# Kernel tuning notes

Measured on AMD Instinct MI355X. Metric: run time of the kernel, lower is better.

Reference implementation:

```python
import jax, jax.numpy as jnp
import numpy as np

DIM = 1024
N_HEADS = 16
HEAD_DIM = DIM // N_HEADS


def setup_inputs() -> dict:
    key = jax.random.key(0)
    ks = jax.random.split(key, 6)
    s = DIM ** -0.5
    return {
        "x": jax.random.normal(ks[0], (2, 2048, DIM), dtype=jnp.float32),
        "Wq": jax.random.normal(ks[1], (DIM, DIM), dtype=jnp.float32) * s,
        "Wk": jax.random.normal(ks[2], (DIM, DIM), dtype=jnp.float32) * s,
        "Wv": jax.random.normal(ks[3], (DIM, DIM), dtype=jnp.float32) * s,
        "Wo": jax.random.normal(ks[4], (DIM, DIM), dtype=jnp.float32) * s,
        "bo": jax.random.normal(ks[5], (DIM,), dtype=jnp.float32) * 0.01,
    }


def reference(x, Wq, Wk, Wv, Wo, bo):
    B, T, C = x.shape
    H, D = N_HEADS, HEAD_DIM
    # Linear(dim, dim, bias=False): y = x @ W^T
    q = (x @ Wq.T).reshape(B, T, H, D).transpose(0, 2, 1, 3)  # B H T D
    k = (x @ Wk.T).reshape(B, T, H, D).transpose(0, 2, 1, 3)
    v = (x @ Wv.T).reshape(B, T, H, D).transpose(0, 2, 1, 3)
    q = q * (D ** -0.5)
    attn = jnp.einsum('bhqd,bhkd->bhqk', q, k)  # B H T T
    causal_mask = jnp.triu(jnp.ones((T, T), dtype=bool), k=1)
    attn = jnp.where(causal_mask, -jnp.inf, attn)
    attn = jax.nn.softmax(attn, axis=-1)
    out = jnp.einsum('bhqk,bhkd->bhqd', attn, v)  # B H T D
    out = out.transpose(0, 2, 1, 3).reshape(B, T, C)
    return out @ Wo.T + bo
```

## Files before the change

### kernel.cpp

```cpp
#include <hip/hip_runtime.h>

typedef __attribute__((ext_vector_type(8))) short bf16x8;
typedef __attribute__((ext_vector_type(4))) float f32x4;

__device__ __forceinline__ ushort f2bf(float f) {
  union { float f; unsigned u; } v; v.f = f;
  unsigned r = v.u + 0x7fffu + ((v.u >> 16) & 1u);
  return (ushort)(r >> 16);
}

__device__ __forceinline__ void g2l16(const void* g, void* l) {
  __builtin_amdgcn_global_load_lds((const __attribute__((address_space(1))) unsigned*)g,
                                   (__attribute__((address_space(3))) unsigned*)l, 16, 0, 0);
}

__global__ __launch_bounds__(256) void cast_x_kernel(const float* __restrict__ x,
                                                     ushort* __restrict__ o, int n4) {
  int i = blockIdx.x * 256 + threadIdx.x;
  if (i >= n4) return;
  float4 v = ((const float4*)x)[i];
  ushort4 u; u.x = f2bf(v.x); u.y = f2bf(v.y); u.z = f2bf(v.z); u.w = f2bf(v.w);
  ((ushort4*)o)[i] = u;
}

__global__ __launch_bounds__(256) void cast_w_kernel(const float* __restrict__ Wq,
                                                     const float* __restrict__ Wk,
                                                     const float* __restrict__ Wv,
                                                     const float* __restrict__ Wo,
                                                     ushort* __restrict__ o) {
  int i = blockIdx.x * 256 + threadIdx.x;
  int row = i >> 8;
  int sel = row >> 10;
  const float* src = (sel == 0) ? Wq : (sel == 1) ? Wk : (sel == 2) ? Wv : Wo;
  float scale = (sel == 0) ? 0.125f : 1.0f;
  float4 v = ((const float4*)src)[i & 0x3FFFF];
  ushort4 u;
  u.x = f2bf(v.x * scale); u.y = f2bf(v.y * scale);
  u.z = f2bf(v.z * scale); u.w = f2bf(v.w * scale);
  ((ushort4*)o)[i] = u;
}

template<bool BF16_OUT, bool BIAS, bool SPLIT>
__global__ __launch_bounds__(256) void gemm_bt(const ushort* __restrict__ A,
                                               const ushort* __restrict__ B,
                                               void* __restrict__ Cout,
                                               const float* __restrict__ bias,
                                               int M, int N, int K) {
  __shared__ __align__(16) ushort As[128 * 32];
  __shared__ __align__(16) ushort Bs[128 * 32];
  const int m0 = blockIdx.y * 128, n0 = blockIdx.x * 128;
  const int tid = threadIdx.x, lane = tid & 63, wid = tid >> 6;
  const int quad = lane >> 4, lc = lane & 15;
  const int wm = (wid >> 1) * 64, wn = (wid & 1) * 64;
  f32x4 acc[4][4] = {};

  const int r0 = wid * 32 + (lane >> 2);
  const int c0 = (lane & 3) * 8;
  const ushort* Ag = A + (size_t)(m0 + r0) * K + c0;
  const ushort* Bg = B + (size_t)(n0 + r0) * K + c0;
  ushort* Al = &As[wid * 1024];
  ushort* Bl = &Bs[wid * 1024];

  for (int k0 = 0; k0 < K; k0 += 32) {
    __syncthreads();
    g2l16(Ag + k0, Al);
    g2l16(Ag + (size_t)16 * K + k0, Al + 512);
    g2l16(Bg + k0, Bl);
    g2l16(Bg + (size_t)16 * K + k0, Bl + 512);
    __syncthreads();

    bf16x8 af[4], bfr[4];
#pragma unroll
    for (int t = 0; t < 4; t++) {
      af[t]  = *(const bf16x8*)&As[(wm + t * 16 + lc) * 32 + quad * 8];
      bfr[t] = *(const bf16x8*)&Bs[(wn + t * 16 + lc) * 32 + quad * 8];
    }
#pragma unroll
    for (int mt = 0; mt < 4; mt++)
#pragma unroll
      for (int nt = 0; nt < 4; nt++)
        acc[mt][nt] = __builtin_amdgcn_mfma_f32_16x16x32_bf16(af[mt], bfr[nt], acc[mt][nt], 0, 0, 0);
  }

#pragma unroll
  for (int mt = 0; mt < 4; mt++) {
#pragma unroll
    for (int r = 0; r < 4; r++) {
      int row = m0 + wm + mt * 16 + quad * 4 + r;
#pragma unroll
      for (int nt = 0; nt < 4; nt++) {
        int col = n0 + wn + nt * 16 + lc;
        float v = acc[mt][nt][r];
        if (BIAS) v += bias[col];
        size_t dst;
        if (SPLIT) dst = ((size_t)(col >> 10) << 22) + (size_t)row * 1024 + (col & 1023);
        else       dst = (size_t)row * N + col;
        if (BF16_OUT) ((ushort*)Cout)[dst] = f2bf(v);
        else          ((float*)Cout)[dst]  = v;
      }
    }
  }
}

__global__ __launch_bounds__(256) void transpose_v(const ushort* __restrict__ Vb,
                                                   ushort* __restrict__ Vt) {
  __shared__ ushort tile[64][72];
  const int bh = blockIdx.y, b = bh >> 4, h = bh & 15;
  const int tt = blockIdx.x;
  const int tid = threadIdx.x;
#pragma unroll
  for (int i = 0; i < 2; i++) {
    int idx = i * 256 + tid;
    int trow = idx >> 3;
    int dcol = (idx & 7) * 8;
    uint4 v = *(const uint4*)(Vb + (size_t)(b * 2048 + tt * 64 + trow) * 1024 + h * 64 + dcol);
    ushort e[8]; *(uint4*)e = v;
#pragma unroll
    for (int j = 0; j < 8; j++) tile[dcol + j][trow] = e[j];
  }
  __syncthreads();
#pragma unroll
  for (int i = 0; i < 2; i++) {
    int idx = i * 256 + tid;
    int drow = idx >> 3;
    int tloc = (idx & 7) * 8;
    uint4 v = *(const uint4*)&tile[drow][tloc];
    *(uint4*)(Vt + (size_t)bh * 131072 + (size_t)drow * 2048 + tt * 64 + tloc) = v;
  }
}

__global__ __launch_bounds__(256) void attn_kernel(const ushort* __restrict__ Qb,
                                                   const ushort* __restrict__ Kb,
                                                   const ushort* __restrict__ Vt,
                                                   ushort* __restrict__ Out) {
  __shared__ __align__(16) ushort Ks[2][64 * 32];
  __shared__ __align__(16) ushort Vs[2][64 * 32];
  __shared__ __align__(16) ushort Ps[4][16][72];

  const int bh = blockIdx.y, b = bh >> 4, h = bh & 15;
  const int qb_block = (int)(gridDim.x - 1 - blockIdx.x) * 64;
  const int tid = threadIdx.x, lane = tid & 63, wid = tid >> 6;
  const int quad = lane >> 4, lc = lane & 15;
  const int qb = qb_block + wid * 16;

  const ushort* Qp = Qb + (size_t)(b * 2048 + qb + lc) * 1024 + h * 64;
  bf16x8 qf0 = *(const bf16x8*)(Qp + quad * 8);
  bf16x8 qf1 = *(const bf16x8*)(Qp + 32 + quad * 8);

  f32x4 o_acc[4] = {};
  float l_r[4] = {0.f, 0.f, 0.f, 0.f};

  const int lrow = lane >> 2, lcol = (lane & 3) * 8;
  const size_t kbase = (size_t)(b * 2048) * 1024 + h * 64;
  const size_t vbase = (size_t)bh * 131072;

  const int ntiles = (qb_block >> 6) + 1;
  for (int kt = 0; kt < ntiles; kt++) {
    const int kb = kt * 64;
    __syncthreads();
#pragma unroll
    for (int cc = 0; cc < 2; cc++) {
      int ck = wid + cc * 4;
      int half = ck >> 2, rg = ck & 3;
      const ushort* gK = Kb + kbase + (size_t)(kb + rg * 16 + lrow) * 1024 + half * 32 + lcol;
      g2l16(gK, &Ks[half][rg * 512]);
      const ushort* gV = Vt + vbase + (size_t)(rg * 16 + lrow) * 2048 + kb + half * 32 + lcol;
      g2l16(gV, &Vs[half][rg * 512]);
    }
    __syncthreads();

    f32x4 s[4];
#pragma unroll
    for (int c = 0; c < 4; c++) {
      bf16x8 kf0 = *(const bf16x8*)&Ks[0][(c * 16 + lc) * 32 + quad * 8];
      bf16x8 kf1 = *(const bf16x8*)&Ks[1][(c * 16 + lc) * 32 + quad * 8];
      f32x4 z = {};
      z = __builtin_amdgcn_mfma_f32_16x16x32_bf16(qf0, kf0, z, 0, 0, 0);
      z = __builtin_amdgcn_mfma_f32_16x16x32_bf16(qf1, kf1, z, 0, 0, 0);
      s[c] = z;
    }

    if (kb + 63 > qb) {
#pragma unroll
      for (int c = 0; c < 4; c++)
#pragma unroll
        for (int r = 0; r < 4; r++) {
          if (kb + c * 16 + lc > qb + quad * 4 + r) s[c][r] = -1e30f;
        }
    }

#pragma unroll
    for (int c = 0; c < 4; c++)
#pragma unroll
      for (int r = 0; r < 4; r++) {
        float p = __expf(s[c][r]);
        l_r[r] += p;
        Ps[wid][quad * 4 + r][c * 16 + lc] = f2bf(p);
      }
    __asm__ volatile("s_waitcnt lgkmcnt(0)" ::: "memory");
    bf16x8 ap0 = *(const bf16x8*)&Ps[wid][lc][quad * 8];
    bf16x8 ap1 = *(const bf16x8*)&Ps[wid][lc][32 + quad * 8];

#pragma unroll
    for (int nt = 0; nt < 4; nt++) {
      bf16x8 vb0 = *(const bf16x8*)&Vs[0][(nt * 16 + lc) * 32 + quad * 8];
      bf16x8 vb1 = *(const bf16x8*)&Vs[1][(nt * 16 + lc) * 32 + quad * 8];
      o_acc[nt] = __builtin_amdgcn_mfma_f32_16x16x32_bf16(ap0, vb0, o_acc[nt], 0, 0, 0);
      o_acc[nt] = __builtin_amdgcn_mfma_f32_16x16x32_bf16(ap1, vb1, o_acc[nt], 0, 0, 0);
    }
  }

#pragma unroll
  for (int r = 0; r < 4; r++) {
    float s_ = l_r[r];
    s_ += __shfl_xor(s_, 1);
    s_ += __shfl_xor(s_, 2);
    s_ += __shfl_xor(s_, 4);
    s_ += __shfl_xor(s_, 8);
    l_r[r] = 1.0f / s_;
  }
#pragma unroll
  for (int r = 0; r < 4; r++) {
    size_t orow = ((size_t)(b * 2048) + qb + quad * 4 + r) * 1024 + h * 64 + lc;
#pragma unroll
    for (int nt = 0; nt < 4; nt++)
      Out[orow + nt * 16] = f2bf(o_acc[nt][r] * l_r[r]);
  }
}

extern "C" void kernel_launch(void* const* d_in, const int* in_sizes, int n_in,
                              void* d_out, int out_size, void* d_ws, size_t ws_size,
                              hipStream_t stream) {
  const float* x  = (const float*)d_in[0];
  const float* Wq = (const float*)d_in[1];
  const float* Wk = (const float*)d_in[2];
  const float* Wv = (const float*)d_in[3];
  const float* Wo = (const float*)d_in[4];
  const float* bo = (const float*)d_in[5];
  float* out = (float*)d_out;

  char* ws = (char*)d_ws;
  ushort* xbf  = (ushort*)(ws);
  ushort* wcat = (ushort*)(ws + (8ull  << 20));
  ushort* qkv  = (ushort*)(ws + (16ull << 20));
  ushort* Vt   = (ushort*)(ws);
  ushort* Qp   = qkv;
  ushort* Kp   = qkv + (1ull << 22);
  ushort* Vp   = qkv + (2ull << 22);
  ushort* attn_out = Vp;

  cast_x_kernel<<<4096, 256, 0, stream>>>(x, xbf, 1048576);
  cast_w_kernel<<<4096, 256, 0, stream>>>(Wq, Wk, Wv, Wo, wcat);

  gemm_bt<true, false, true><<<dim3(24, 32), 256, 0, stream>>>(
      xbf, wcat, qkv, nullptr, 4096, 3072, 1024);

  transpose_v<<<dim3(32, 32), 256, 0, stream>>>(Vp, Vt);

  attn_kernel<<<dim3(32, 32), 256, 0, stream>>>(Qp, Kp, Vt, attn_out);

  gemm_bt<false, true, false><<<dim3(8, 32), 256, 0, stream>>>(
      attn_out, wcat + (size_t)3072 * 1024, out, bo, 4096, 1024, 1024);
}
```

Before: 224.1 us.

## Double-buffer GEMM and attention loads, widen attention q-tile, use exp2

GEMM now double-buffers its LDS tiles so the next K-slice loads while MFMAs run, and the output projection uses a 128x64 tile to launch more blocks. Attention processes 128 query rows per block (32 per wave), double-buffers K/V tiles, balances causal work by interleaving short and long blocks, and folds log2(e) into the Wq scale so the kernel can use exp2f. bf16 rounding is simplified to round-half-up, which slightly changes numerics. Double buffering has only one barrier per iteration, so correctness depends on the async load into the other buffer being ordered behind that barrier.

```diff
diff --git a/kernel.cpp b/kernel.cpp
--- a/kernel.cpp
+++ b/kernel.cpp
@@ -1,12 +1,12 @@
 #include <hip/hip_runtime.h>
+#include <math.h>
 
 typedef __attribute__((ext_vector_type(8))) short bf16x8;
 typedef __attribute__((ext_vector_type(4))) float f32x4;
 
 __device__ __forceinline__ ushort f2bf(float f) {
   union { float f; unsigned u; } v; v.f = f;
-  unsigned r = v.u + 0x7fffu + ((v.u >> 16) & 1u);
-  return (ushort)(r >> 16);
+  return (ushort)((v.u + 0x8000u) >> 16);
 }
 
 __device__ __forceinline__ void g2l16(const void* g, void* l) {
@@ -32,7 +32,7 @@
   int row = i >> 8;
   int sel = row >> 10;
   const float* src = (sel == 0) ? Wq : (sel == 1) ? Wk : (sel == 2) ? Wv : Wo;
-  float scale = (sel == 0) ? 0.125f : 1.0f;
+  float scale = (sel == 0) ? 0.125f * 1.44269504088896f : 1.0f;
   float4 v = ((const float4*)src)[i & 0x3FFFF];
   ushort4 u;
   u.x = f2bf(v.x * scale); u.y = f2bf(v.y * scale);
@@ -40,50 +40,60 @@
   ((ushort4*)o)[i] = u;
 }
 
-template<bool BF16_OUT, bool BIAS, bool SPLIT>
+template<int BN, bool BF16_OUT, bool BIAS, bool SPLIT>
 __global__ __launch_bounds__(256) void gemm_bt(const ushort* __restrict__ A,
                                                const ushort* __restrict__ B,
                                                void* __restrict__ Cout,
                                                const float* __restrict__ bias,
                                                int M, int N, int K) {
-  __shared__ __align__(16) ushort As[128 * 32];
-  __shared__ __align__(16) ushort Bs[128 * 32];
-  const int m0 = blockIdx.y * 128, n0 = blockIdx.x * 128;
+  __shared__ __align__(16) ushort As[2][128 * 32];
+  __shared__ __align__(16) ushort Bs[2][BN * 32];
+  const int m0 = blockIdx.y * 128, n0 = blockIdx.x * BN;
   const int tid = threadIdx.x, lane = tid & 63, wid = tid >> 6;
   const int quad = lane >> 4, lc = lane & 15;
-  const int wm = (wid >> 1) * 64, wn = (wid & 1) * 64;
-  f32x4 acc[4][4] = {};
-
-  const int r0 = wid * 32 + (lane >> 2);
-  const int c0 = (lane & 3) * 8;
-  const ushort* Ag = A + (size_t)(m0 + r0) * K + c0;
-  const ushort* Bg = B + (size_t)(n0 + r0) * K + c0;
-  ushort* Al = &As[wid * 1024];
-  ushort* Bl = &Bs[wid * 1024];
-
+  const int lrow = lane >> 2, lcol = (lane & 3) * 8;
+  const int wm = (BN == 128) ? (wid >> 1) * 64 : wid * 32;
+  const int wn = (BN == 128) ? (wid & 1) * 64 : 0;
+  constexpr int MT = (BN == 128) ? 4 : 2;
+
+  f32x4 acc[MT][4] = {};
+
+  auto stage = [&](int k0, int nb) {
+    const ushort* Ag = A + (size_t)(m0 + wid * 32 + lrow) * K + k0 + lcol;
+    g2l16(Ag, &As[nb][wid * 1024]);
+    g2l16(Ag + (size_t)16 * K, &As[nb][wid * 1024 + 512]);
+    if constexpr (BN == 128) {
+      const ushort* Bg = B + (size_t)(n0 + wid * 32 + lrow) * K + k0 + lcol;
+      g2l16(Bg, &Bs[nb][wid * 1024]);
+      g2l16(Bg + (size_t)16 * K, &Bs[nb][wid * 1024 + 512]);
+    } else {
+      const ushort* Bg = B + (size_t)(n0 + wid * 16 + lrow) * K + k0 + lcol;
+      g2l16(Bg, &Bs[nb][wid * 512]);
+    }
+  };
+
+  stage(0, 0);
   for (int k0 = 0; k0 < K; k0 += 32) {
+    const int nb = (k0 >> 5) & 1;
     __syncthreads();
-    g2l16(Ag + k0, Al);
-    g2l16(Ag + (size_t)16 * K + k0, Al + 512);
-    g2l16(Bg + k0, Bl);
-    g2l16(Bg + (size_t)16 * K + k0, Bl + 512);
-    __syncthreads();
-
-    bf16x8 af[4], bfr[4];
-#pragma unroll
-    for (int t = 0; t < 4; t++) {
-      af[t]  = *(const bf16x8*)&As[(wm + t * 16 + lc) * 32 + quad * 8];
-      bfr[t] = *(const bf16x8*)&Bs[(wn + t * 16 + lc) * 32 + quad * 8];
-    }
-#pragma unroll
-    for (int mt = 0; mt < 4; mt++)
+    if (k0 + 32 < K) stage(k0 + 32, nb ^ 1);
+
+    bf16x8 af[MT], bfr[4];
+#pragma unroll
+    for (int t = 0; t < MT; t++)
+      af[t] = *(const bf16x8*)&As[nb][(wm + t * 16 + lc) * 32 + quad * 8];
+#pragma unroll
+    for (int t = 0; t < 4; t++)
+      bfr[t] = *(const bf16x8*)&Bs[nb][(wn + t * 16 + lc) * 32 + quad * 8];
+#pragma unroll
+    for (int mt = 0; mt < MT; mt++)
 #pragma unroll
       for (int nt = 0; nt < 4; nt++)
         acc[mt][nt] = __builtin_amdgcn_mfma_f32_16x16x32_bf16(af[mt], bfr[nt], acc[mt][nt], 0, 0, 0);
   }
 
 #pragma unroll
-  for (int mt = 0; mt < 4; mt++) {
+  for (int mt = 0; mt < MT; mt++) {
 #pragma unroll
     for (int r = 0; r < 4; r++) {
       int row = m0 + wm + mt * 16 + quad * 4 + r;
@@ -129,103 +139,114 @@
   }
 }
 
-__global__ __launch_bounds__(256) void attn_kernel(const ushort* __restrict__ Qb,
-                                                   const ushort* __restrict__ Kb,
-                                                   const ushort* __restrict__ Vt,
-                                                   ushort* __restrict__ Out) {
-  __shared__ __align__(16) ushort Ks[2][64 * 32];
-  __shared__ __align__(16) ushort Vs[2][64 * 32];
-  __shared__ __align__(16) ushort Ps[4][16][72];
+__global__ __launch_bounds__(256, 2) void attn_kernel(const ushort* __restrict__ Qb,
+                                                      const ushort* __restrict__ Kb,
+                                                      const ushort* __restrict__ Vt,
+                                                      ushort* __restrict__ Out) {
+  __shared__ __align__(16) ushort Ks[2][2][64 * 32];
+  __shared__ __align__(16) ushort Vs[2][2][64 * 32];
+  __shared__ __align__(16) ushort Ps[4][32][72];
 
   const int bh = blockIdx.y, b = bh >> 4, h = bh & 15;
-  const int qb_block = (int)(gridDim.x - 1 - blockIdx.x) * 64;
+  const int bx = blockIdx.x;
+  const int ord = (bx & 1) ? (bx >> 1) : (15 - (bx >> 1));
+  const int qb_block = ord * 128;
   const int tid = threadIdx.x, lane = tid & 63, wid = tid >> 6;
   const int quad = lane >> 4, lc = lane & 15;
-  const int qb = qb_block + wid * 16;
-
-  const ushort* Qp = Qb + (size_t)(b * 2048 + qb + lc) * 1024 + h * 64;
-  bf16x8 qf0 = *(const bf16x8*)(Qp + quad * 8);
-  bf16x8 qf1 = *(const bf16x8*)(Qp + 32 + quad * 8);
-
-  f32x4 o_acc[4] = {};
-  float l_r[4] = {0.f, 0.f, 0.f, 0.f};
-
   const int lrow = lane >> 2, lcol = (lane & 3) * 8;
+  const int qbw = qb_block + wid * 32;
+
   const size_t kbase = (size_t)(b * 2048) * 1024 + h * 64;
   const size_t vbase = (size_t)bh * 131072;
 
-  const int ntiles = (qb_block >> 6) + 1;
+  bf16x8 qf[2][2];
+#pragma unroll
+  for (int t = 0; t < 2; t++) {
+    const ushort* Qp = Qb + kbase + (size_t)(qbw + t * 16 + lc) * 1024;
+    qf[t][0] = *(const bf16x8*)(Qp + quad * 8);
+    qf[t][1] = *(const bf16x8*)(Qp + 32 + quad * 8);
+  }
+
+  f32x4 o_acc[2][4] = {};
+  float l_r[2][4] = {};
+
+  auto stage = [&](int kb, int nb) {
+    const ushort* gK = Kb + kbase + (size_t)(kb + wid * 16 + lrow) * 1024 + lcol;
+    g2l16(gK,      &Ks[nb][0][wid * 512]);
+    g2l16(gK + 32, &Ks[nb][1][wid * 512]);
+    const ushort* gV = Vt + vbase + (size_t)(wid * 16 + lrow) * 2048 + kb + lcol;
+    g2l16(gV,      &Vs[nb][0][wid * 512]);
+    g2l16(gV + 32, &Vs[nb][1][wid * 512]);
+  };
+
+  const int ntiles = (qb_block >> 6) + 2;
+  stage(0, 0);
   for (int kt = 0; kt < ntiles; kt++) {
     const int kb = kt * 64;
+    const int buf = kt & 1;
     __syncthreads();
-#pragma unroll
-    for (int cc = 0; cc < 2; cc++) {
-      int ck = wid + cc * 4;
-      int half = ck >> 2, rg = ck & 3;
-      const ushort* gK = Kb + kbase + (size_t)(kb + rg * 16 + lrow) * 1024 + half * 32 + lcol;
-      g2l16(gK, &Ks[half][rg * 512]);
-      const ushort* gV = Vt + vbase + (size_t)(rg * 16 + lrow) * 2048 + kb + half * 32 + lcol;
-      g2l16(gV, &Vs[half][rg * 512]);
-    }
-    __syncthreads();
-
-    f32x4 s[4];
+    if (kt + 1 < ntiles) stage(kb + 64, buf ^ 1);
+
 #pragma unroll
     for (int c = 0; c < 4; c++) {
-      bf16x8 kf0 = *(const bf16x8*)&Ks[0][(c * 16 + lc) * 32 + quad * 8];
-      bf16x8 kf1 = *(const bf16x8*)&Ks[1][(c * 16 + lc) * 32 + quad * 8];
-      f32x4 z = {};
-      z = __builtin_amdgcn_mfma_f32_16x16x32_bf16(qf0, kf0, z, 0, 0, 0);
-      z = __builtin_amdgcn_mfma_f32_16x16x32_bf16(qf1, kf1, z, 0, 0, 0);
-      s[c] = z;
-    }
-
-    if (kb + 63 > qb) {
-#pragma unroll
-      for (int c = 0; c < 4; c++)
+      bf16x8 kf0 = *(const bf16x8*)&Ks[buf][0][(c * 16 + lc) * 32 + quad * 8];
+      bf16x8 kf1 = *(const bf16x8*)&Ks[buf][1][(c * 16 + lc) * 32 + quad * 8];
+#pragma unroll
+      for (int t = 0; t < 2; t++) {
+        f32x4 z = {};
+        z = __builtin_amdgcn_mfma_f32_16x16x32_bf16(qf[t][0], kf0, z, 0, 0, 0);
+        z = __builtin_amdgcn_mfma_f32_16x16x32_bf16(qf[t][1], kf1, z, 0, 0, 0);
+        const bool diag = (kb + 63 > qbw + t * 16);
 #pragma unroll
         for (int r = 0; r < 4; r++) {
-          if (kb + c * 16 + lc > qb + quad * 4 + r) s[c][r] = -1e30f;
+          float sv = z[r];
+          if (diag && (kb + c * 16 + lc > qbw + t * 16 + quad * 4 + r)) sv = -1e30f;
+          float pv = exp2f(sv);
+          l_r[t][r] += pv;
+          Ps[wid][t * 16 + quad * 4 + r][c * 16 + lc] = f2bf(pv);
         }
-    }
-
-#pragma unroll
-    for (int c = 0; c < 4; c++)
-#pragma unroll
-      for (int r = 0; r < 4; r++) {
-        float p = __expf(s[c][r]);
-        l_r[r] += p;
-        Ps[wid][quad * 4 + r][c * 16 + lc] = f2bf(p);
       }
+    }
     __asm__ volatile("s_waitcnt lgkmcnt(0)" ::: "memory");
-    bf16x8 ap0 = *(const bf16x8*)&Ps[wid][lc][quad * 8];
-    bf16x8 ap1 = *(const bf16x8*)&Ps[wid][lc][32 + quad * 8];
-
+
+    bf16x8 ap[2][2];
+#pragma unroll
+    for (int t = 0; t < 2; t++) {
+      ap[t][0] = *(const bf16x8*)&Ps[wid][t * 16 + lc][quad * 8];
+      ap[t][1] = *(const bf16x8*)&Ps[wid][t * 16 + lc][32 + quad * 8];
+    }
 #pragma unroll
     for (int nt = 0; nt < 4; nt++) {
-      bf16x8 vb0 = *(const bf16x8*)&Vs[0][(nt * 16 + lc) * 32 + quad * 8];
-      bf16x8 vb1 = *(const bf16x8*)&Vs[1][(nt * 16 + lc) * 32 + quad * 8];
-      o_acc[nt] = __builtin_amdgcn_mfma_f32_16x16x32_bf16(ap0, vb0, o_acc[nt], 0, 0, 0);
-      o_acc[nt] = __builtin_amdgcn_mfma_f32_16x16x32_bf16(ap1, vb1, o_acc[nt], 0, 0, 0);
-    }
-  }
-
-#pragma unroll
-  for (int r = 0; r < 4; r++) {
-    float s_ = l_r[r];
-    s_ += __shfl_xor(s_, 1);
-    s_ += __shfl_xor(s_, 2);
-    s_ += __shfl_xor(s_, 4);
-    s_ += __shfl_xor(s_, 8);
-    l_r[r] = 1.0f / s_;
-  }
-#pragma unroll
-  for (int r = 0; r < 4; r++) {
-    size_t orow = ((size_t)(b * 2048) + qb + quad * 4 + r) * 1024 + h * 64 + lc;
-#pragma unroll
-    for (int nt = 0; nt < 4; nt++)
-      Out[orow + nt * 16] = f2bf(o_acc[nt][r] * l_r[r]);
-  }
+      bf16x8 vb0 = *(const bf16x8*)&Vs[buf][0][(nt * 16 + lc) * 32 + quad * 8];
+      bf16x8 vb1 = *(const bf16x8*)&Vs[buf][1][(nt * 16 + lc) * 32 + quad * 8];
+#pragma unroll
+      for (int t = 0; t < 2; t++) {
+        o_acc[t][nt] = __builtin_amdgcn_mfma_f32_16x16x32_bf16(ap[t][0], vb0, o_acc[t][nt], 0, 0, 0);
+        o_acc[t][nt] = __builtin_amdgcn_mfma_f32_16x16x32_bf16(ap[t][1], vb1, o_acc[t][nt], 0, 0, 0);
+      }
+    }
+  }
+
+#pragma unroll
+  for (int t = 0; t < 2; t++)
+#pragma unroll
+    for (int r = 0; r < 4; r++) {
+      float s_ = l_r[t][r];
+      s_ += __shfl_xor(s_, 1);
+      s_ += __shfl_xor(s_, 2);
+      s_ += __shfl_xor(s_, 4);
+      s_ += __shfl_xor(s_, 8);
+      l_r[t][r] = 1.0f / s_;
+    }
+#pragma unroll
+  for (int t = 0; t < 2; t++)
+#pragma unroll
+    for (int r = 0; r < 4; r++) {
+      size_t orow = ((size_t)(b * 2048) + qbw + t * 16 + quad * 4 + r) * 1024 + h * 64 + lc;
+#pragma unroll
+      for (int nt = 0; nt < 4; nt++)
+        Out[orow + nt * 16] = f2bf(o_acc[t][nt][r] * l_r[t][r]);
+    }
 }
 
 extern "C" void kernel_launch(void* const* d_in, const int* in_sizes, int n_in,
@@ -252,13 +273,13 @@
   cast_x_kernel<<<4096, 256, 0, stream>>>(x, xbf, 1048576);
   cast_w_kernel<<<4096, 256, 0, stream>>>(Wq, Wk, Wv, Wo, wcat);
 
-  gemm_bt<true, false, true><<<dim3(24, 32), 256, 0, stream>>>(
+  gemm_bt<128, true, false, true><<<dim3(24, 32), 256, 0, stream>>>(
       xbf, wcat, qkv, nullptr, 4096, 3072, 1024);
 
   transpose_v<<<dim3(32, 32), 256, 0, stream>>>(Vp, Vt);
 
-  attn_kernel<<<dim3(32, 32), 256, 0, stream>>>(Qp, Kp, Vt, attn_out);
-
-  gemm_bt<false, true, false><<<dim3(8, 32), 256, 0, stream>>>(
+  attn_kernel<<<dim3(16, 32), 256, 0, stream>>>(Qp, Kp, Vt, attn_out);
+
+  gemm_bt<64, false, true, false><<<dim3(16, 32), 256, 0, stream>>>(
       attn_out, wcat + (size_t)3072 * 1024, out, bo, 4096, 1024, 1024);
 }
```

After: 229.1 us. 2.2% more time.
